# Kernel optimization log

Measured on AMD Instinct MI355X. Metric: run time of the kernel, lower is better.

Reference implementation:

```python
import jax, jax.numpy as jnp
import numpy as np

B, K, D = 8192, 32, 256

def setup_inputs() -> dict:
    key = jax.random.key(0)
    ks = jax.random.split(key, 8)
    embedded_state = jax.random.normal(ks[0], (B, 1, D), dtype=jnp.float32)
    eps = jax.random.normal(ks[1], (B, 1, D), dtype=jnp.float32)
    W_mu = 0.02 * jax.random.normal(ks[2], (D, D), dtype=jnp.float32)
    b_mu = jnp.zeros((D,), dtype=jnp.float32)
    W_sig = 0.02 * jax.random.normal(ks[3], (D, D), dtype=jnp.float32)
    b_sig = jnp.zeros((D,), dtype=jnp.float32)
    mu_c = jax.random.uniform(ks[4], (K, D), dtype=jnp.float32)
    log_sigma_sq_c = jnp.zeros((K, D), dtype=jnp.float32)
    return {"embedded_state": embedded_state, "eps": eps, "W_mu": W_mu, "b_mu": b_mu,
            "W_sig": W_sig, "b_sig": b_sig, "mu_c": mu_c, "log_sigma_sq_c": log_sigma_sq_c}

def reference(embedded_state, eps, W_mu, b_mu, W_sig, b_sig, mu_c, log_sigma_sq_c):
    # linear projections (torch Linear: x @ W.T + b)
    mu_z = jnp.einsum('bnd,ed->bne', embedded_state, W_mu) + b_mu          # [B,1,D]
    log_sigma_sq_z = jnp.einsum('bnd,ed->bne', embedded_state, W_sig) + b_sig  # [B,1,D]
    z = mu_z + jnp.sqrt(jnp.exp(log_sigma_sq_z)) * eps                      # [B,1,D]
    inv_sig_c = jnp.exp(-log_sigma_sq_c)                                    # [K,D]
    # cluster-distance logits: broadcast [B,1,D] vs [K,D] -> [B,K,D] -> sum D
    pi_logits = -jnp.sum((z - mu_c[None]) ** 2 * inv_sig_c[None], axis=-1)  # [B,K]
    pi_post = jax.nn.softmax(pi_logits, axis=-1) + 1e-10                    # [B,K]
    # GMM loss terms (original code implicitly broadcasts pi_post over D)
    a = log_sigma_sq_c[None] + jnp.exp(log_sigma_sq_z) * inv_sig_c[None]    # [B,K,D]
    b = (mu_z - mu_c[None]) ** 2 * inv_sig_c[None]                          # [B,K,D]
    c = a + b
    batch_gaussian_loss = 0.5 * jnp.sum(pi_post[:, :, None] * c)
    mean_pi = jnp.mean(pi_post, axis=0)                                     # [K]
    batch_uniform_loss = jnp.mean(mean_pi * jnp.log(mean_pi))
    return z, batch_gaussian_loss, batch_uniform_loss
```

## Files before the change

### kernel.cpp

```cpp
#include <hip/hip_runtime.h>
#include <hip/hip_bf16.h>

typedef __attribute__((ext_vector_type(4))) float f32x4;
typedef __attribute__((ext_vector_type(8))) short short8;

#define NB 8192
#define ND 256
#define NK 32
#define PADF 520

static __device__ __forceinline__ unsigned short f2bf(float f) {
  return __builtin_bit_cast(unsigned short, __float2bfloat16(f));
}

static __device__ __forceinline__ f32x4 mfma_bf16(short8 a, short8 b, f32x4 c) {
  return __builtin_amdgcn_mfma_f32_16x16x32_bf16(a, b, c, 0, 0, 0);
}

static __device__ __forceinline__ short8 pack_bf16x8(float4 lo, float4 hi) {
  short8 r;
  r[0] = (short)f2bf(lo.x); r[1] = (short)f2bf(lo.y);
  r[2] = (short)f2bf(lo.z); r[3] = (short)f2bf(lo.w);
  r[4] = (short)f2bf(hi.x); r[5] = (short)f2bf(hi.y);
  r[6] = (short)f2bf(hi.z); r[7] = (short)f2bf(hi.w);
  return r;
}

__global__ __launch_bounds__(256) void prep_k(const float* __restrict__ wmu,
                                              const float* __restrict__ wsig,
                                              __hip_bfloat16* __restrict__ wsw,
                                              const float* __restrict__ mu_c,
                                              const float* __restrict__ lsc,
                                              __hip_bfloat16* __restrict__ bcsw,
                                              float* __restrict__ c3k,
                                              float* __restrict__ ckk) {
  __shared__ float red1[4], red2[4];
  const int blk = blockIdx.x, tid = threadIdx.x;
  if (blk < 512) {
    int i = blk * 256 + tid;
    int f = i >> 9, r = i & 511;
    int l = r >> 3, e = r & 7;
    int n = (f >> 3) * 16 + (l & 15);
    int k = (f & 7) * 32 + ((l >> 4) << 3) + e;
    float v = (n < 256) ? wmu[n * ND + k] : wsig[(n - 256) * ND + k];
    wsw[i] = __float2bfloat16(v);
  } else {
    int k = blk - 512;
    int d = tid;
    float l = lsc[k * ND + d];
    float inv = __expf(-l);
    float mc = mu_c[k * ND + d];
    const int rb = k >> 4, lrow = k & 15;
    {
      int c = d;
      int kb = c >> 5, q = (c >> 3) & 3, e = c & 7;
      bcsw[(size_t)(rb * 16 + kb) * 512 + (q * 16 + lrow) * 8 + e] = __float2bfloat16(inv);
    }
    {
      int c = 256 + d;
      int kb = c >> 5, q = (c >> 3) & 3, e = c & 7;
      bcsw[(size_t)(rb * 16 + kb) * 512 + (q * 16 + lrow) * 8 + e] = __float2bfloat16(-2.f * mc * inv);
    }
    float s1 = l, s2 = mc * mc * inv;
    #pragma unroll
    for (int sh = 32; sh; sh >>= 1) { s1 += __shfl_xor(s1, sh); s2 += __shfl_xor(s2, sh); }
    int lane = tid & 63, wv = tid >> 6;
    if (lane == 0) { red1[wv] = s1; red2[wv] = s2; }
    __syncthreads();
    if (tid == 0) {
      float t1 = red1[0] + red1[1] + red1[2] + red1[3];
      float t2 = red2[0] + red2[1] + red2[2] + red2[3];
      c3k[k] = t2;
      ckk[k] = t1 + t2;
    }
  }
}

__global__ __launch_bounds__(256, 2) void mega_k(const float* __restrict__ xf,
                                                 const __hip_bfloat16* __restrict__ wsw,
                                                 const float* __restrict__ bmu,
                                                 const float* __restrict__ bsigv,
                                                 const float* __restrict__ eps,
                                                 const __hip_bfloat16* __restrict__ bcsw,
                                                 const float* __restrict__ c3k,
                                                 const float* __restrict__ ckk,
                                                 float* __restrict__ zout,
                                                 float* __restrict__ part) {
  __shared__ __align__(16) unsigned short AcT[16][PADF];
  __shared__ __align__(16) unsigned short AqT[16][PADF];
  __shared__ __align__(16) char uniBuf[16896];
  __shared__ float piP[NK];
  __shared__ float gSum;
  unsigned short (*Axb)[264] = (unsigned short (*)[264])uniBuf;
  float (*sW)[2][16][33] = (float (*)[2][16][33])uniBuf;

  const int tid = threadIdx.x, lane = tid & 63, w = tid >> 6;
  const int lrow = lane & 15, q = lane >> 4;
  const int m0 = blockIdx.x * 16;

  if (tid < NK) piP[tid] = 0.f;
  if (tid == NK) gSum = 0.f;

  {
    const int r = tid >> 4, c0 = (tid & 15) * 16;
    const float* xr = xf + (size_t)(m0 + r) * ND + c0;
    float4 a0 = *reinterpret_cast<const float4*>(xr);
    float4 a1 = *reinterpret_cast<const float4*>(xr + 4);
    float4 a2 = *reinterpret_cast<const float4*>(xr + 8);
    float4 a3 = *reinterpret_cast<const float4*>(xr + 12);
    *reinterpret_cast<short8*>(&Axb[r][c0])     = pack_bf16x8(a0, a1);
    *reinterpret_cast<short8*>(&Axb[r][c0 + 8]) = pack_bf16x8(a2, a3);
  }
  __syncthreads();

  short8 aF[8];
  #pragma unroll
  for (int kk = 0; kk < 8; ++kk)
    aF[kk] = *reinterpret_cast<const short8*>(&Axb[lrow][kk * 32 + q * 8]);

  #pragma unroll
  for (int r = 0; r < 4; ++r) {
    const int rb = r * 4 + w;
    const __hip_bfloat16* pM = wsw + (size_t)(rb * 8) * 512 + lane * 8;
    const __hip_bfloat16* pS = wsw + (size_t)((16 + rb) * 8) * 512 + lane * 8;
    short8 bM[8], bS[8];
    #pragma unroll
    for (int kk = 0; kk < 8; ++kk) {
      bM[kk] = *reinterpret_cast<const short8*>(pM + kk * 512);
      bS[kk] = *reinterpret_cast<const short8*>(pS + kk * 512);
    }
    f32x4 aM = (f32x4){0.f, 0.f, 0.f, 0.f};
    f32x4 aS = (f32x4){0.f, 0.f, 0.f, 0.f};
    #pragma unroll
    for (int kk = 0; kk < 8; ++kk) {
      aM = mfma_bf16(aF[kk], bM[kk], aM);
      aS = mfma_bf16(aF[kk], bS[kk], aS);
    }
    const int d = rb * 16 + lrow;
    const float bm = bmu[d], bs = bsigv[d];
    #pragma unroll
    for (int j = 0; j < 4; ++j) {
      const int bl = q * 4 + j;
      const int b = m0 + bl;
      float muv = aM[j] + bm;
      float lsv = aS[j] + bs;
      float sq  = __expf(lsv);
      float e   = eps[(size_t)b * ND + d];
      float zv  = muv + sqrtf(sq) * e;
      zout[(size_t)b * ND + d] = zv;
      AcT[bl][d]       = f2bf(zv * zv);
      AcT[bl][256 + d] = f2bf(zv);
      AqT[bl][d]       = f2bf(sq + muv * muv);
      AqT[bl][256 + d] = f2bf(muv);
    }
  }
  __syncthreads();

  f32x4 cL[2], cQ[2];
  cL[0] = cL[1] = cQ[0] = cQ[1] = (f32x4){0.f, 0.f, 0.f, 0.f};
  {
    short8 b0v[4], b1v[4], acv[4], aqv[4];
    #pragma unroll
    for (int ks = 0; ks < 4; ++ks) {
      const int kb = w * 4 + ks;
      b0v[ks] = *reinterpret_cast<const short8*>(bcsw + (size_t)kb * 512 + lane * 8);
      b1v[ks] = *reinterpret_cast<const short8*>(bcsw + (size_t)(16 + kb) * 512 + lane * 8);
      const int kc = kb * 32 + q * 8;
      acv[ks] = *reinterpret_cast<const short8*>(&AcT[lrow][kc]);
      aqv[ks] = *reinterpret_cast<const short8*>(&AqT[lrow][kc]);
    }
    #pragma unroll
    for (int ks = 0; ks < 4; ++ks) {
      cL[0] = mfma_bf16(acv[ks], b0v[ks], cL[0]);
      cL[1] = mfma_bf16(acv[ks], b1v[ks], cL[1]);
      cQ[0] = mfma_bf16(aqv[ks], b0v[ks], cQ[0]);
      cQ[1] = mfma_bf16(aqv[ks], b1v[ks], cQ[1]);
    }
  }
  #pragma unroll
  for (int nfk = 0; nfk < 2; ++nfk)
    #pragma unroll
    for (int j = 0; j < 4; ++j) {
      sW[w][0][q * 4 + j][nfk * 16 + lrow] = cL[nfk][j];
      sW[w][1][q * 4 + j][nfk * 16 + lrow] = cQ[nfk][j];
    }
  __syncthreads();

  {
    const int b = tid >> 4, kk = tid & 15;
    float L0 = sW[0][0][b][kk]      + sW[1][0][b][kk]      + sW[2][0][b][kk]      + sW[3][0][b][kk];
    float L1 = sW[0][0][b][kk + 16] + sW[1][0][b][kk + 16] + sW[2][0][b][kk + 16] + sW[3][0][b][kk + 16];
    float Q0 = sW[0][1][b][kk]      + sW[1][1][b][kk]      + sW[2][1][b][kk]      + sW[3][1][b][kk];
    float Q1 = sW[0][1][b][kk + 16] + sW[1][1][b][kk + 16] + sW[2][1][b][kk + 16] + sW[3][1][b][kk + 16];
    float l0 = -(L0 + c3k[kk]);
    float l1 = -(L1 + c3k[kk + 16]);
    float mx = fmaxf(l0, l1);
    #pragma unroll
    for (int s = 8; s; s >>= 1) mx = fmaxf(mx, __shfl_xor(mx, s));
    float p0 = __expf(l0 - mx), p1 = __expf(l1 - mx);
    float ps = p0 + p1;
    #pragma unroll
    for (int s = 8; s; s >>= 1) ps += __shfl_xor(ps, s);
    float pi0 = p0 / ps + 1e-10f;
    float pi1 = p1 / ps + 1e-10f;
    float g = pi0 * (Q0 + ckk[kk]) + pi1 * (Q1 + ckk[kk + 16]);
    #pragma unroll
    for (int s = 8; s; s >>= 1) g += __shfl_xor(g, s);
    atomicAdd(&piP[kk], pi0);
    atomicAdd(&piP[kk + 16], pi1);
    if (kk == 0) atomicAdd(&gSum, g);
  }
  __syncthreads();
  if (tid < NK)  part[(size_t)tid * 512 + blockIdx.x] = piP[tid];
  if (tid == NK) part[(size_t)NK * 512 + blockIdx.x] = 0.5f * gSum;
}

__global__ __launch_bounds__(256) void final_k(const float* __restrict__ part,
                                               float* __restrict__ out) {
  __shared__ double red[4][33];
  const int tid = threadIdx.x, lane = tid & 63, wv = tid >> 6;
  if (lane < 33) {
    const float4* p4 = reinterpret_cast<const float4*>(part + (size_t)lane * 512);
    double acc = 0.0;
    for (int i = wv * 32; i < wv * 32 + 32; ++i) {
      float4 v = p4[i];
      acc += (double)v.x + (double)v.y + (double)v.z + (double)v.w;
    }
    red[wv][lane] = acc;
  }
  __syncthreads();
  if (tid >= 64) return;
  double s = (tid < 33) ? (red[0][tid] + red[1][tid] + red[2][tid] + red[3][tid]) : 0.0;
  if (tid == 32) out[NB * ND] = (float)s;
  double t = 0.0;
  if (tid < 32) { double mk = s / (double)NB; t = mk * log(mk); }
  #pragma unroll
  for (int sh = 16; sh; sh >>= 1) t += __shfl_xor(t, sh);
  if (tid == 0) out[NB * ND + 1] = (float)(t / (double)NK);
}

extern "C" void kernel_launch(void* const* d_in, const int* in_sizes, int n_in,
                              void* d_out, int out_size, void* d_ws, size_t ws_size,
                              hipStream_t stream) {
  const float* x    = (const float*)d_in[0];
  const float* eps  = (const float*)d_in[1];
  const float* wmu  = (const float*)d_in[2];
  const float* bmu  = (const float*)d_in[3];
  const float* wsig = (const float*)d_in[4];
  const float* bsig = (const float*)d_in[5];
  const float* mu_c = (const float*)d_in[6];
  const float* lsc  = (const float*)d_in[7];
  float* out = (float*)d_out;

  char* ws = (char*)d_ws;
  __hip_bfloat16* wsw  = (__hip_bfloat16*)ws;
  __hip_bfloat16* bcsw = (__hip_bfloat16*)(ws + (256u << 10));
  float* c3k  = (float*)(ws + (288u << 10));
  float* ckk  = (float*)(ws + (288u << 10) + 256u);
  float* part = (float*)(ws + (288u << 10) + 512u);

  prep_k<<<544, 256, 0, stream>>>(wmu, wsig, wsw, mu_c, lsc, bcsw, c3k, ckk);
  mega_k<<<512, 256, 0, stream>>>(x, wsw, bmu, bsig, eps, bcsw, c3k, ckk, out, part);
  final_k<<<1, 256, 0, stream>>>(part, out);
}
```

Before: 26.18 us.

## Double mega kernel block to 512 threads and prefetch eps/bias early

Raises the mega kernel from 4 to 8 waves per block, so each wave handles half as many output column tiles in the projection GEMM and half as many K-chunks in the cluster-distance MFMAs. The cross-wave reduction buffer doubles to match. Eps and bias values are loaded at kernel start so their latency overlaps the x load and bf16 packing. The projection loop is split so the mu and sigma weight fragments are loaded in sequence, which lowers register pressure for the tighter launch bounds. The costs are more LDS per block, a larger cross-wave reduction, and more registers held live for the prefetched values.

```diff
diff --git a/kernel.cpp b/kernel.cpp
--- a/kernel.cpp
+++ b/kernel.cpp
@@ -76,7 +76,7 @@
   }
 }
 
-__global__ __launch_bounds__(256, 2) void mega_k(const float* __restrict__ xf,
+__global__ __launch_bounds__(512, 4) void mega_k(const float* __restrict__ xf,
                                                  const __hip_bfloat16* __restrict__ wsw,
                                                  const float* __restrict__ bmu,
                                                  const float* __restrict__ bsigv,
@@ -88,7 +88,7 @@
                                                  float* __restrict__ part) {
   __shared__ __align__(16) unsigned short AcT[16][PADF];
   __shared__ __align__(16) unsigned short AqT[16][PADF];
-  __shared__ __align__(16) char uniBuf[16896];
+  __shared__ __align__(16) char uniBuf[33792];
   __shared__ float piP[NK];
   __shared__ float gSum;
   unsigned short (*Axb)[264] = (unsigned short (*)[264])uniBuf;
@@ -101,15 +101,23 @@
   if (tid < NK) piP[tid] = 0.f;
   if (tid == NK) gSum = 0.f;
 
+  float bmv[2], bsv[2], epv[2][4];
+  #pragma unroll
+  for (int r = 0; r < 2; ++r) {
+    const int d = (r * 8 + w) * 16 + lrow;
+    bmv[r] = bmu[d];
+    bsv[r] = bsigv[d];
+    #pragma unroll
+    for (int j = 0; j < 4; ++j)
+      epv[r][j] = eps[(size_t)(m0 + q * 4 + j) * ND + d];
+  }
+
   {
-    const int r = tid >> 4, c0 = (tid & 15) * 16;
+    const int r = tid >> 5, c0 = (tid & 31) * 8;
     const float* xr = xf + (size_t)(m0 + r) * ND + c0;
     float4 a0 = *reinterpret_cast<const float4*>(xr);
     float4 a1 = *reinterpret_cast<const float4*>(xr + 4);
-    float4 a2 = *reinterpret_cast<const float4*>(xr + 8);
-    float4 a3 = *reinterpret_cast<const float4*>(xr + 12);
-    *reinterpret_cast<short8*>(&Axb[r][c0])     = pack_bf16x8(a0, a1);
-    *reinterpret_cast<short8*>(&Axb[r][c0 + 8]) = pack_bf16x8(a2, a3);
+    *reinterpret_cast<short8*>(&Axb[r][c0]) = pack_bf16x8(a0, a1);
   }
   __syncthreads();
 
@@ -119,34 +127,39 @@
     aF[kk] = *reinterpret_cast<const short8*>(&Axb[lrow][kk * 32 + q * 8]);
 
   #pragma unroll
-  for (int r = 0; r < 4; ++r) {
-    const int rb = r * 4 + w;
+  for (int r = 0; r < 2; ++r) {
+    const int rb = r * 8 + w;
     const __hip_bfloat16* pM = wsw + (size_t)(rb * 8) * 512 + lane * 8;
     const __hip_bfloat16* pS = wsw + (size_t)((16 + rb) * 8) * 512 + lane * 8;
-    short8 bM[8], bS[8];
-    #pragma unroll
-    for (int kk = 0; kk < 8; ++kk) {
-      bM[kk] = *reinterpret_cast<const short8*>(pM + kk * 512);
-      bS[kk] = *reinterpret_cast<const short8*>(pS + kk * 512);
-    }
     f32x4 aM = (f32x4){0.f, 0.f, 0.f, 0.f};
     f32x4 aS = (f32x4){0.f, 0.f, 0.f, 0.f};
-    #pragma unroll
-    for (int kk = 0; kk < 8; ++kk) {
-      aM = mfma_bf16(aF[kk], bM[kk], aM);
-      aS = mfma_bf16(aF[kk], bS[kk], aS);
+    {
+      short8 bM[8];
+      #pragma unroll
+      for (int kk = 0; kk < 8; ++kk)
+        bM[kk] = *reinterpret_cast<const short8*>(pM + kk * 512);
+      #pragma unroll
+      for (int kk = 0; kk < 8; ++kk)
+        aM = mfma_bf16(aF[kk], bM[kk], aM);
+    }
+    {
+      short8 bS[8];
+      #pragma unroll
+      for (int kk = 0; kk < 8; ++kk)
+        bS[kk] = *reinterpret_cast<const short8*>(pS + kk * 512);
+      #pragma unroll
+      for (int kk = 0; kk < 8; ++kk)
+        aS = mfma_bf16(aF[kk], bS[kk], aS);
     }
     const int d = rb * 16 + lrow;
-    const float bm = bmu[d], bs = bsigv[d];
     #pragma unroll
     for (int j = 0; j < 4; ++j) {
       const int bl = q * 4 + j;
       const int b = m0 + bl;
-      float muv = aM[j] + bm;
-      float lsv = aS[j] + bs;
+      float muv = aM[j] + bmv[r];
+      float lsv = aS[j] + bsv[r];
       float sq  = __expf(lsv);
-      float e   = eps[(size_t)b * ND + d];
-      float zv  = muv + sqrtf(sq) * e;
+      float zv  = muv + sqrtf(sq) * epv[r][j];
       zout[(size_t)b * ND + d] = zv;
       AcT[bl][d]       = f2bf(zv * zv);
       AcT[bl][256 + d] = f2bf(zv);
@@ -159,10 +172,10 @@
   f32x4 cL[2], cQ[2];
   cL[0] = cL[1] = cQ[0] = cQ[1] = (f32x4){0.f, 0.f, 0.f, 0.f};
   {
-    short8 b0v[4], b1v[4], acv[4], aqv[4];
-    #pragma unroll
-    for (int ks = 0; ks < 4; ++ks) {
-      const int kb = w * 4 + ks;
+    short8 b0v[2], b1v[2], acv[2], aqv[2];
+    #pragma unroll
+    for (int ks = 0; ks < 2; ++ks) {
+      const int kb = w * 2 + ks;
       b0v[ks] = *reinterpret_cast<const short8*>(bcsw + (size_t)kb * 512 + lane * 8);
       b1v[ks] = *reinterpret_cast<const short8*>(bcsw + (size_t)(16 + kb) * 512 + lane * 8);
       const int kc = kb * 32 + q * 8;
@@ -170,7 +183,7 @@
       aqv[ks] = *reinterpret_cast<const short8*>(&AqT[lrow][kc]);
     }
     #pragma unroll
-    for (int ks = 0; ks < 4; ++ks) {
+    for (int ks = 0; ks < 2; ++ks) {
       cL[0] = mfma_bf16(acv[ks], b0v[ks], cL[0]);
       cL[1] = mfma_bf16(acv[ks], b1v[ks], cL[1]);
       cQ[0] = mfma_bf16(aqv[ks], b0v[ks], cQ[0]);
@@ -186,12 +199,14 @@
     }
   __syncthreads();
 
-  {
+  if (tid < 256) {
     const int b = tid >> 4, kk = tid & 15;
-    float L0 = sW[0][0][b][kk]      + sW[1][0][b][kk]      + sW[2][0][b][kk]      + sW[3][0][b][kk];
-    float L1 = sW[0][0][b][kk + 16] + sW[1][0][b][kk + 16] + sW[2][0][b][kk + 16] + sW[3][0][b][kk + 16];
-    float Q0 = sW[0][1][b][kk]      + sW[1][1][b][kk]      + sW[2][1][b][kk]      + sW[3][1][b][kk];
-    float Q1 = sW[0][1][b][kk + 16] + sW[1][1][b][kk + 16] + sW[2][1][b][kk + 16] + sW[3][1][b][kk + 16];
+    float L0 = 0.f, L1 = 0.f, Q0 = 0.f, Q1 = 0.f;
+    #pragma unroll
+    for (int ww = 0; ww < 8; ++ww) {
+      L0 += sW[ww][0][b][kk];      L1 += sW[ww][0][b][kk + 16];
+      Q0 += sW[ww][1][b][kk];      Q1 += sW[ww][1][b][kk + 16];
+    }
     float l0 = -(L0 + c3k[kk]);
     float l1 = -(L1 + c3k[kk + 16]);
     float mx = fmaxf(l0, l1);
@@ -260,6 +275,6 @@
   float* part = (float*)(ws + (288u << 10) + 512u);
 
   prep_k<<<544, 256, 0, stream>>>(wmu, wsig, wsw, mu_c, lsc, bcsw, c3k, ckk);
-  mega_k<<<512, 256, 0, stream>>>(x, wsw, bmu, bsig, eps, bcsw, c3k, ckk, out, part);
+  mega_k<<<512, 512, 0, stream>>>(x, wsw, bmu, bsig, eps, bcsw, c3k, ckk, out, part);
   final_k<<<1, 256, 0, stream>>>(part, out);
 }
```

Result: no change. 26.18 us (+0.0%).
